# Kernel optimization log

Measured on AMD Instinct MI355X. Metric: run time of the kernel, lower is better.

## Reference

```python
import jax, jax.numpy as jnp
import numpy as np
import math

BS, H, L, D = 4, 8, 1024, 64
P = 513  # max_path_num + 1


def setup_inputs() -> dict:
    key = jax.random.key(0)
    ks = jax.random.split(key, 6)
    return {
        "query": jax.random.normal(ks[0], (BS, H, L, D), dtype=jnp.float32),
        "key": jax.random.normal(ks[1], (BS, H, L, D), dtype=jnp.float32),
        "value": jax.random.normal(ks[2], (BS, H, L, D), dtype=jnp.float32),
        "relation": jax.random.normal(ks[3], (BS, P, D), dtype=jnp.float32),
        "path_map": jax.random.randint(ks[4], (BS, L, L), 0, P, dtype=jnp.int32),
        "mask": jax.random.randint(ks[5], (BS, 1, L, L), 0, 2, dtype=jnp.int32),
    }


def reference(query, key, value, relation, path_map, mask):
    bs, h, Lc, d = query.shape
    p = relation.shape[1]
    # content score: bs,h,L,L
    score = jnp.einsum("bhik,bhjk->bhij", query, key)
    # relation score. Torch gathers with index of shape (bs,1,L,L) from a
    # (bs,h,L,P) tensor, which reads head 0 only and broadcasts over heads.
    score_r_h0 = jnp.einsum("bik,bpk->bip", query[:, 0], relation)  # bs,L,P
    gathered = jnp.take_along_axis(score_r_h0, path_map, axis=-1)   # bs,L,L
    score = score + gathered[:, None, :, :]
    scores = score / math.sqrt(d)
    scores = jnp.where(mask == 0, jnp.float32(-1e9), scores)
    p_attn = jax.nn.softmax(scores, axis=-1)  # bs,h,L,L
    attn_sum = jnp.einsum("bhij,bhjk->bhik", p_attn, value)
    # scatter-add attention probs into relation buckets: bs,h,L,P
    b_ix = jnp.arange(bs)[:, None, None, None]
    h_ix = jnp.arange(h)[None, :, None, None]
    i_ix = jnp.arange(Lc)[None, None, :, None]
    pm = jnp.broadcast_to(path_map[:, None, :, :], (bs, h, Lc, Lc))
    r_buckets = jnp.zeros((bs, h, Lc, p), dtype=p_attn.dtype).at[b_ix, h_ix, i_ix, pm].add(p_attn)
    r_attn_sum = jnp.einsum("bhip,bpk->bhik", r_buckets, relation)
    attn_sum = attn_sum + r_attn_sum
    return (attn_sum, p_attn)
```

## Files before the change

### kernel.cpp

```cpp
#include <hip/hip_runtime.h>


#define BSZ 4
#define NH 8
#define LSEQ 1024
#define DH 64
#define NP 513
#define TI 16
#define NT 1024
#define SRX 545
#define RTC 544

#define NQE (BSZ*NH*LSEQ*DH)
#define NRE (BSZ*NP*DH)
#define NRT (BSZ*DH*RTC)
#define OFF_QH 0
#define OFF_QL (NQE)
#define OFF_KH (2*NQE)
#define OFF_KL (3*NQE)
#define OFF_VT (4*NQE)
#define OFF_RH (5*NQE)
#define OFF_RL (5*NQE + NRE)
#define OFF_RT (5*NQE + 2*NRE)
#define WS_NEED ((size_t)(5*(size_t)NQE + 2*(size_t)NRE + (size_t)NRT) * 2)

typedef __attribute__((ext_vector_type(8))) short bf16x8;
typedef __attribute__((ext_vector_type(4))) float f32x4;
typedef __attribute__((ext_vector_type(4))) ushort u16x4;

__device__ __forceinline__ ushort f2bf(float x) {
    uint u = __float_as_uint(x);
    u += 0x7FFFu + ((u >> 16) & 1u);
    return (ushort)(u >> 16);
}
__device__ __forceinline__ float bf2f(ushort h) {
    return __uint_as_float(((uint)h) << 16);
}


__global__ void prep_qk(const float* __restrict__ Q, const float* __restrict__ K,
                        ushort* __restrict__ ws) {
    const int n4 = NQE / 4;
    for (int i = blockIdx.x * blockDim.x + threadIdx.x; i < 2 * n4;
         i += gridDim.x * blockDim.x) {
        int isK = i >= n4;
        int base = i - isK * n4;
        float4 v = ((const float4*)(isK ? K : Q))[base];
        float xs[4] = {v.x, v.y, v.z, v.w};
        u16x4 hh, ll;
        #pragma unroll
        for (int e = 0; e < 4; ++e) {
            ushort hi = f2bf(xs[e]);
            hh[e] = hi;
            ll[e] = f2bf(xs[e] - bf2f(hi));
        }
        *(u16x4*)(ws + (isK ? OFF_KH : OFF_QH) + (size_t)base * 4) = hh;
        *(u16x4*)(ws + (isK ? OFF_KL : OFF_QL) + (size_t)base * 4) = ll;
    }
}

__global__ void prep_rel(const float* __restrict__ REL, ushort* __restrict__ ws) {
    const int tot = NRE + NRT;
    for (int i = blockIdx.x * blockDim.x + threadIdx.x; i < tot;
         i += gridDim.x * blockDim.x) {
        if (i < NRE) {
            float x = REL[i];
            ushort hi = f2bf(x);
            ws[OFF_RH + i] = hi;
            ws[OFF_RL + i] = f2bf(x - bf2f(hi));
        } else {
            int j = i - NRE;
            int b = j / (DH * RTC);
            int r = j - b * (DH * RTC);
            int d = r / RTC;
            int p = r - d * RTC;
            float x = (p < NP) ? REL[((size_t)b * NP + p) * DH + d] : 0.f;
            ws[OFF_RT + j] = f2bf(x);
        }
    }
}

__global__ void prep_vt(const float* __restrict__ V, ushort* __restrict__ ws) {
    for (int i = blockIdx.x * blockDim.x + threadIdx.x; i < NQE;
         i += gridDim.x * blockDim.x) {
        int bh = i >> 16;
        int r  = i & 65535;
        int d  = r >> 10;
        int j  = r & 1023;
        ws[OFF_VT + (size_t)i] = f2bf(V[((size_t)bh << 16) + (j << 6) + d]);
    }
}


__global__ __launch_bounds__(NT, 4) void raa_main(
    const ushort* __restrict__ ws,
    const int* __restrict__ PM, const int* __restrict__ MASK,
    float* __restrict__ OUT_A, float* __restrict__ OUT_P)
{
    __shared__ float  X[TI * SRX];
    __shared__ ushort sPb[TI * 1024];
    __shared__ float  sAttn[TI * DH];
    __shared__ float  sRed[16 * 17];
    __shared__ float  sFin[16];

    const int tid = threadIdx.x;
    const int w  = tid >> 6;
    const int l  = tid & 63;
    const int lg = l >> 4;
    const int lm = l & 15;

    const int it = blockIdx.x, h = blockIdx.y, b = blockIdx.z;
    const int i0 = it * TI;
    const int bh = b * NH + h;

    const ushort* Qh  = ws + OFF_QH + (size_t)bh * LSEQ * DH;
    const ushort* Ql  = ws + OFF_QL + (size_t)bh * LSEQ * DH;
    const ushort* Q0h = ws + OFF_QH + (size_t)b * NH * LSEQ * DH;
    const ushort* Q0l = ws + OFF_QL + (size_t)b * NH * LSEQ * DH;
    const ushort* Kh  = ws + OFF_KH + (size_t)bh * LSEQ * DH;
    const ushort* Kl  = ws + OFF_KL + (size_t)bh * LSEQ * DH;
    const ushort* Vt  = ws + OFF_VT + (size_t)bh * DH * LSEQ;
    const ushort* Rh  = ws + OFF_RH + (size_t)b * NP * DH;
    const ushort* Rl  = ws + OFF_RL + (size_t)b * NP * DH;
    const ushort* Rt  = ws + OFF_RT + (size_t)b * DH * RTC;
    const int* PMb = PM + (size_t)b * LSEQ * LSEQ;
    const int* MKb = MASK + (size_t)b * LSEQ * LSEQ;

    sAttn[tid] = 0.f;

    bf16x8 q0h[2], q0l[2], qhh[2], qhl[2];
    #pragma unroll
    for (int ks = 0; ks < 2; ++ks) {
        size_t ao = (size_t)(i0 + lm) * DH + ks * 32 + lg * 8;
        q0h[ks] = *(const bf16x8*)(Q0h + ao);
        q0l[ks] = *(const bf16x8*)(Q0l + ao);
        qhh[ks] = *(const bf16x8*)(Qh + ao);
        qhl[ks] = *(const bf16x8*)(Ql + ao);
    }

    int pmr[16], mkr[16];
    #pragma unroll
    for (int t = 0; t < 4; ++t) {
        #pragma unroll
        for (int e = 0; e < 4; ++e) {
            int col = (4 * w + t) * 16 + lm;
            int row = 4 * lg + e;
            size_t off = (size_t)(i0 + row) * LSEQ + col;
            pmr[t * 4 + e] = PMb[off];
            mkr[t * 4 + e] = MKb[off];
        }
    }

    for (int ct = w; ct < 33; ct += 16) {
        int p0 = ct * 16;
        int prow = p0 + lm; if (prow > 512) prow = 512;
        f32x4 a0 = {0.f, 0.f, 0.f, 0.f};
        #pragma unroll
        for (int ks = 0; ks < 2; ++ks) {
            size_t bo = (size_t)prow * DH + ks * 32 + lg * 8;
            bf16x8 bh8 = *(const bf16x8*)(Rh + bo);
            bf16x8 bl8 = *(const bf16x8*)(Rl + bo);
            a0 = __builtin_amdgcn_mfma_f32_16x16x32_bf16(q0h[ks], bh8, a0, 0, 0, 0);
            a0 = __builtin_amdgcn_mfma_f32_16x16x32_bf16(q0l[ks], bh8, a0, 0, 0, 0);
            a0 = __builtin_amdgcn_mfma_f32_16x16x32_bf16(q0h[ks], bl8, a0, 0, 0, 0);
        }
        if (p0 + lm < NP) {
            #pragma unroll
            for (int e = 0; e < 4; ++e)
                X[(4 * lg + e) * SRX + p0 + lm] = a0[e];
        }
    }

    f32x4 acc[4];
    #pragma unroll
    for (int t = 0; t < 4; ++t) {
        int j0 = (4 * w + t) * 16;
        acc[t] = (f32x4){0.f, 0.f, 0.f, 0.f};
        #pragma unroll
        for (int ks = 0; ks < 2; ++ks) {
            size_t bo = (size_t)(j0 + lm) * DH + ks * 32 + lg * 8;
            bf16x8 kh8 = *(const bf16x8*)(Kh + bo);
            bf16x8 kl8 = *(const bf16x8*)(Kl + bo);
            acc[t] = __builtin_amdgcn_mfma_f32_16x16x32_bf16(qhh[ks], kh8, acc[t], 0, 0, 0);
            acc[t] = __builtin_amdgcn_mfma_f32_16x16x32_bf16(qhl[ks], kh8, acc[t], 0, 0, 0);
            acc[t] = __builtin_amdgcn_mfma_f32_16x16x32_bf16(qhh[ks], kl8, acc[t], 0, 0, 0);
        }
    }
    __syncthreads();

    #pragma unroll
    for (int t = 0; t < 4; ++t) {
        #pragma unroll
        for (int e = 0; e < 4; ++e) {
            int row = 4 * lg + e;
            float g = X[row * SRX + pmr[t * 4 + e]];
            acc[t][e] = (mkr[t * 4 + e] == 0) ? -1e9f : (acc[t][e] + g) * 0.125f;
        }
    }
    __syncthreads();
    for (int idx = tid; idx < TI * SRX; idx += NT) X[idx] = 0.f;
    __syncthreads();

    float Mr[4];
    #pragma unroll
    for (int e = 0; e < 4; ++e) {
        float m = fmaxf(fmaxf(acc[0][e], acc[1][e]), fmaxf(acc[2][e], acc[3][e]));
        #pragma unroll
        for (int o = 8; o >= 1; o >>= 1) m = fmaxf(m, __shfl_xor(m, o));
        Mr[e] = m;
    }
    if (lm == 0) {
        #pragma unroll
        for (int e = 0; e < 4; ++e) sRed[(4 * lg + e) * 17 + w] = Mr[e];
    }
    __syncthreads();
    if (w == 0 && l < 16) {
        float m = -INFINITY;
        for (int ww = 0; ww < 16; ++ww) m = fmaxf(m, sRed[l * 17 + ww]);
        sFin[l] = m;
    }
    __syncthreads();
    #pragma unroll
    for (int e = 0; e < 4; ++e) Mr[e] = sFin[4 * lg + e];

    float Sr[4];
    #pragma unroll
    for (int e = 0; e < 4; ++e) {
        float s = 0.f;
        #pragma unroll
        for (int t = 0; t < 4; ++t) {
            float v = __expf(acc[t][e] - Mr[e]);
            acc[t][e] = v;
            s += v;
        }
        #pragma unroll
        for (int o = 8; o >= 1; o >>= 1) s += __shfl_xor(s, o);
        Sr[e] = s;
    }
    if (lm == 0) {
        #pragma unroll
        for (int e = 0; e < 4; ++e) sRed[(4 * lg + e) * 17 + w] = Sr[e];
    }
    __syncthreads();
    if (w == 0 && l < 16) {
        float s = 0.f;
        for (int ww = 0; ww < 16; ++ww) s += sRed[l * 17 + ww];
        sFin[l] = s;
    }
    __syncthreads();

    float inv[4];
    #pragma unroll
    for (int e = 0; e < 4; ++e) inv[e] = 1.0f / sFin[4 * lg + e];

    const size_t pbase = (((size_t)bh) * LSEQ + i0) * LSEQ;
    #pragma unroll
    for (int t = 0; t < 4; ++t) {
        int col = (4 * w + t) * 16 + lm;
        #pragma unroll
        for (int e = 0; e < 4; ++e) {
            int row = 4 * lg + e;
            float p = acc[t][e] * inv[e];
            OUT_P[pbase + (size_t)row * LSEQ + col] = p;
            sPb[row * 1024 + (((col >> 3) ^ (row & 7)) << 3) + (col & 7)] = f2bf(p);
            atomicAdd(&X[row * SRX + pmr[t * 4 + e]], p);
        }
    }
    __syncthreads();

    if (w < 8) {
        int ct = w >> 1, jh = w & 1;
        int d0 = ct * 16;
        f32x4 pa = {0.f, 0.f, 0.f, 0.f};
        #pragma unroll 4
        for (int ks = 0; ks < 16; ++ks) {
            int j0 = jh * 512 + ks * 32;
            int ch = (j0 >> 3) + lg;
            bf16x8 a = *(const bf16x8*)&sPb[lm * 1024 + ((ch ^ (lm & 7)) << 3)];
            bf16x8 bb = *(const bf16x8*)(Vt + (size_t)(d0 + lm) * LSEQ + j0 + lg * 8);
            pa = __builtin_amdgcn_mfma_f32_16x16x32_bf16(a, bb, pa, 0, 0, 0);
        }
        #pragma unroll
        for (int e = 0; e < 4; ++e)
            atomicAdd(&sAttn[(4 * lg + e) * DH + d0 + lm], pa[e]);
    } else {
        int ct = (w - 8) >> 1, ph = w & 1;
        int d0 = ct * 16;
        int nks = ph ? 8 : 9;
        int pb0 = ph ? 288 : 0;
        f32x4 pa = {0.f, 0.f, 0.f, 0.f};
        for (int ks = 0; ks < nks; ++ks) {
            int p0 = pb0 + ks * 32;
            bf16x8 a;
            #pragma unroll
            for (int e = 0; e < 8; ++e)
                a[e] = (short)f2bf(X[lm * SRX + p0 + lg * 8 + e]);
            bf16x8 bb = *(const bf16x8*)(Rt + (size_t)(d0 + lm) * RTC + p0 + lg * 8);
            pa = __builtin_amdgcn_mfma_f32_16x16x32_bf16(a, bb, pa, 0, 0, 0);
        }
        #pragma unroll
        for (int e = 0; e < 4; ++e)
            atomicAdd(&sAttn[(4 * lg + e) * DH + d0 + lm], pa[e]);
    }
    __syncthreads();

    OUT_A[(((size_t)bh) * LSEQ + i0 + (tid >> 6)) * DH + (tid & 63)] = sAttn[tid];
}


__global__ __launch_bounds__(NT, 4) void raa_fallback(
    const float* __restrict__ Q, const float* __restrict__ K,
    const float* __restrict__ V, const float* __restrict__ REL,
    const int* __restrict__ PM, const int* __restrict__ MASK,
    float* __restrict__ OUT_A, float* __restrict__ OUT_P)
{
    __shared__ ushort sQh[TI * 64];
    __shared__ ushort sQl[TI * 64];
    __shared__ float  sR[TI * NP];
    __shared__ ushort sPb[TI * 1024];
    __shared__ float  sAttn[TI * 64];
    __shared__ float  sRed[16 * 17];
    __shared__ float  sFin[16];

    const int tid = threadIdx.x;
    const int w  = tid >> 6;
    const int l  = tid & 63;
    const int lg = l >> 4;
    const int lm = l & 15;

    const int it = blockIdx.x, h = blockIdx.y, b = blockIdx.z;
    const int i0 = it * TI;

    const float* Qb0  = Q + ((size_t)b * NH + 0) * LSEQ * DH;
    const float* Qbh  = Q + ((size_t)b * NH + h) * LSEQ * DH;
    const float* Kbh  = K + ((size_t)b * NH + h) * LSEQ * DH;
    const float* Vbh  = V + ((size_t)b * NH + h) * LSEQ * DH;
    const float* RELb = REL + (size_t)b * NP * DH;
    const int*   PMb  = PM  + (size_t)b * LSEQ * LSEQ;
    const int*   MKb  = MASK + (size_t)b * LSEQ * LSEQ;

    {
        int row = tid >> 6, kk = tid & 63;
        float x = Qb0[(size_t)(i0 + row) * DH + kk];
        ushort hi = f2bf(x);
        ushort lo = f2bf(x - bf2f(hi));
        int ad = row * 64 + (((kk >> 3) ^ (row & 7)) << 3) + (kk & 7);
        sQh[ad] = hi; sQl[ad] = lo;
        sAttn[tid] = 0.f;
    }
    __syncthreads();

    bf16x8 qh[2], ql[2];
    #pragma unroll
    for (int ks = 0; ks < 2; ++ks) {
        int ch = lg + 4 * ks;
        int ad = lm * 64 + ((ch ^ (lm & 7)) << 3);
        qh[ks] = *(const bf16x8*)&sQh[ad];
        ql[ks] = *(const bf16x8*)&sQl[ad];
    }
    __syncthreads();

    {
        int row = tid >> 6, kk = tid & 63;
        float x = Qbh[(size_t)(i0 + row) * DH + kk];
        ushort hi = f2bf(x);
        ushort lo = f2bf(x - bf2f(hi));
        int ad = row * 64 + (((kk >> 3) ^ (row & 7)) << 3) + (kk & 7);
        sQh[ad] = hi; sQl[ad] = lo;
    }

    for (int ct = w; ct < 33; ct += 16) {
        int p0 = ct * 16;
        int prow = p0 + lm; if (prow > 512) prow = 512;
        const float* bsrc = RELb + (size_t)prow * DH + 8 * lg;
        f32x4 acc = {0.f, 0.f, 0.f, 0.f};
        #pragma unroll
        for (int ks = 0; ks < 2; ++ks) {
            float4 v0 = *(const float4*)(bsrc + ks * 32);
            float4 v1 = *(const float4*)(bsrc + ks * 32 + 4);
            float xs[8] = {v0.x, v0.y, v0.z, v0.w, v1.x, v1.y, v1.z, v1.w};
            bf16x8 bh, bl;
            #pragma unroll
            for (int e = 0; e < 8; ++e) {
                ushort hi = f2bf(xs[e]);
                bh[e] = (short)hi;
                bl[e] = (short)f2bf(xs[e] - bf2f(hi));
            }
            acc = __builtin_amdgcn_mfma_f32_16x16x32_bf16(qh[ks], bh, acc, 0, 0, 0);
            acc = __builtin_amdgcn_mfma_f32_16x16x32_bf16(ql[ks], bh, acc, 0, 0, 0);
            acc = __builtin_amdgcn_mfma_f32_16x16x32_bf16(qh[ks], bl, acc, 0, 0, 0);
        }
        int pcol = p0 + lm;
        if (pcol < NP) {
            #pragma unroll
            for (int e = 0; e < 4; ++e)
                sR[(4 * lg + e) * NP + pcol] = acc[e];
        }
    }
    __syncthreads();

    {
        int ad0;
        #pragma unroll
        for (int ks = 0; ks < 2; ++ks) {
            int ch = lg + 4 * ks;
            ad0 = lm * 64 + ((ch ^ (lm & 7)) << 3);
            qh[ks] = *(const bf16x8*)&sQh[ad0];
            ql[ks] = *(const bf16x8*)&sQl[ad0];
        }
    }
    f32x4 acc[4];
    #pragma unroll
    for (int t = 0; t < 4; ++t) {
        int j = (4 * w + t) * 16 + lm;
        const float* bsrc = Kbh + (size_t)j * DH + 8 * lg;
        acc[t] = (f32x4){0.f, 0.f, 0.f, 0.f};
        #pragma unroll
        for (int ks = 0; ks < 2; ++ks) {
            float4 v0 = *(const float4*)(bsrc + ks * 32);
            float4 v1 = *(const float4*)(bsrc + ks * 32 + 4);
            float xs[8] = {v0.x, v0.y, v0.z, v0.w, v1.x, v1.y, v1.z, v1.w};
            bf16x8 bh, bl;
            #pragma unroll
            for (int e = 0; e < 8; ++e) {
                ushort hi = f2bf(xs[e]);
                bh[e] = (short)hi;
                bl[e] = (short)f2bf(xs[e] - bf2f(hi));
            }
            acc[t] = __builtin_amdgcn_mfma_f32_16x16x32_bf16(qh[ks], bh, acc[t], 0, 0, 0);
            acc[t] = __builtin_amdgcn_mfma_f32_16x16x32_bf16(ql[ks], bh, acc[t], 0, 0, 0);
            acc[t] = __builtin_amdgcn_mfma_f32_16x16x32_bf16(qh[ks], bl, acc[t], 0, 0, 0);
        }
    }

    #pragma unroll
    for (int t = 0; t < 4; ++t) {
        int col = (4 * w + t) * 16 + lm;
        #pragma unroll
        for (int e = 0; e < 4; ++e) {
            int row = 4 * lg + e;
            size_t off = (size_t)(i0 + row) * LSEQ + col;
            int pm = PMb[off];
            int mk = MKb[off];
            float g = sR[row * NP + pm];
            acc[t][e] = (mk == 0) ? -1e9f : (acc[t][e] + g) * 0.125f;
        }
    }
    __syncthreads();
    for (int idx = tid; idx < TI * NP; idx += NT) sR[idx] = 0.f;
    __syncthreads();

    float Mr[4];
    #pragma unroll
    for (int e = 0; e < 4; ++e) {
        float m = fmaxf(fmaxf(acc[0][e], acc[1][e]), fmaxf(acc[2][e], acc[3][e]));
        #pragma unroll
        for (int o = 8; o >= 1; o >>= 1) m = fmaxf(m, __shfl_xor(m, o));
        Mr[e] = m;
    }
    if (lm == 0) {
        #pragma unroll
        for (int e = 0; e < 4; ++e) sRed[(4 * lg + e) * 17 + w] = Mr[e];
    }
    __syncthreads();
    if (w == 0 && l < 16) {
        float m = -INFINITY;
        for (int ww = 0; ww < 16; ++ww) m = fmaxf(m, sRed[l * 17 + ww]);
        sFin[l] = m;
    }
    __syncthreads();
    #pragma unroll
    for (int e = 0; e < 4; ++e) Mr[e] = sFin[4 * lg + e];

    float Sr[4];
    #pragma unroll
    for (int e = 0; e < 4; ++e) {
        float s = 0.f;
        #pragma unroll
        for (int t = 0; t < 4; ++t) {
            float v = __expf(acc[t][e] - Mr[e]);
            acc[t][e] = v;
            s += v;
        }
        #pragma unroll
        for (int o = 8; o >= 1; o >>= 1) s += __shfl_xor(s, o);
        Sr[e] = s;
    }
    if (lm == 0) {
        #pragma unroll
        for (int e = 0; e < 4; ++e) sRed[(4 * lg + e) * 17 + w] = Sr[e];
    }
    __syncthreads();
    if (w == 0 && l < 16) {
        float s = 0.f;
        for (int ww = 0; ww < 16; ++ww) s += sRed[l * 17 + ww];
        sFin[l] = s;
    }
    __syncthreads();

    float inv[4];
    #pragma unroll
    for (int e = 0; e < 4; ++e) inv[e] = 1.0f / sFin[4 * lg + e];

    const size_t pbase = (((size_t)b * NH + h) * LSEQ + i0) * LSEQ;
    #pragma unroll
    for (int t = 0; t < 4; ++t) {
        int col = (4 * w + t) * 16 + lm;
        #pragma unroll
        for (int e = 0; e < 4; ++e) {
            int row = 4 * lg + e;
            float p = acc[t][e] * inv[e];
            OUT_P[pbase + (size_t)row * LSEQ + col] = p;
            int ad = row * 1024 + (((col >> 3) ^ (row & 7)) << 3) + (col & 7);
            sPb[ad] = f2bf(p);
            int pm = PMb[(size_t)(i0 + row) * LSEQ + col];
            atomicAdd(&sR[row * NP + pm], p);
        }
    }
    __syncthreads();

    if (w < 8) {
        int ct = w >> 1, jh = w & 1;
        int d = ct * 16 + lm;
        f32x4 pa = {0.f, 0.f, 0.f, 0.f};
        for (int ks = 0; ks < 16; ++ks) {
            int j0 = jh * 512 + ks * 32;
            int ch = (j0 >> 3) + lg;
            bf16x8 a = *(const bf16x8*)&sPb[lm * 1024 + ((ch ^ (lm & 7)) << 3)];
            const float* vs = Vbh + (size_t)(j0 + 8 * lg) * DH + d;
            bf16x8 bb;
            #pragma unroll
            for (int e = 0; e < 8; ++e) bb[e] = (short)f2bf(vs[(size_t)e * DH]);
            pa = __builtin_amdgcn_mfma_f32_16x16x32_bf16(a, bb, pa, 0, 0, 0);
        }
        #pragma unroll
        for (int e = 0; e < 4; ++e)
            atomicAdd(&sAttn[(4 * lg + e) * 64 + d], pa[e]);
    } else {
        int ct = (w - 8) >> 1, ph = w & 1;
        int d = ct * 16 + lm;
        int nks = ph ? 9 : 8;
        f32x4 pa = {0.f, 0.f, 0.f, 0.f};
        for (int ks = 0; ks < nks; ++ks) {
            int p0 = ph * 256 + ks * 32 + 8 * lg;
            bf16x8 a, bb;
            #pragma unroll
            for (int e = 0; e < 8; ++e) {
                int pp = p0 + e;
                float av = (pp < NP) ? sR[lm * NP + pp] : 0.f;
                a[e] = (short)f2bf(av);
                int pc = (pp < NP) ? pp : (NP - 1);
                bb[e] = (short)f2bf(RELb[(size_t)pc * DH + d]);
            }
            pa = __builtin_amdgcn_mfma_f32_16x16x32_bf16(a, bb, pa, 0, 0, 0);
        }
        #pragma unroll
        for (int e = 0; e < 4; ++e)
            atomicAdd(&sAttn[(4 * lg + e) * 64 + d], pa[e]);
    }
    __syncthreads();

    {
        int row = tid >> 6, col = tid & 63;
        OUT_A[(((size_t)b * NH + h) * LSEQ + i0 + row) * DH + col] =
            sAttn[row * 64 + col];
    }
}

extern "C" void kernel_launch(void* const* d_in, const int* in_sizes, int n_in,
                              void* d_out, int out_size, void* d_ws, size_t ws_size,
                              hipStream_t stream) {
    const float* q    = (const float*)d_in[0];
    const float* k    = (const float*)d_in[1];
    const float* v    = (const float*)d_in[2];
    const float* rel  = (const float*)d_in[3];
    const int*   pm   = (const int*)d_in[4];
    const int*   mask = (const int*)d_in[5];
    float* out_a = (float*)d_out;
    float* out_p = (float*)d_out + (size_t)BSZ * NH * LSEQ * DH;

    dim3 grid(LSEQ / TI, NH, BSZ);
    if (ws_size >= WS_NEED && d_ws != nullptr) {
        ushort* ws = (ushort*)d_ws;
        prep_qk<<<2048, 256, 0, stream>>>(q, k, ws);
        prep_rel<<<512, 256, 0, stream>>>(rel, ws);
        prep_vt<<<2048, 256, 0, stream>>>(v, ws);
        raa_main<<<grid, NT, 0, stream>>>((const ushort*)ws, pm, mask, out_a, out_p);
    } else {
        raa_fallback<<<grid, NT, 0, stream>>>(q, k, v, rel, pm, mask, out_a, out_p);
    }
}
```

Baseline: 585.8 us.

## Precompute relation scores once per batch and streamline softmax and output stores

```diff
diff --git a/kernel.cpp b/kernel.cpp
--- a/kernel.cpp
+++ b/kernel.cpp
@@ -12,17 +12,16 @@
 #define RTC 544
 
 #define NQE (BSZ*NH*LSEQ*DH)
-#define NRE (BSZ*NP*DH)
 #define NRT (BSZ*DH*RTC)
+#define NSR (BSZ*LSEQ*NP)
 #define OFF_QH 0
 #define OFF_QL (NQE)
 #define OFF_KH (2*NQE)
 #define OFF_KL (3*NQE)
 #define OFF_VT (4*NQE)
-#define OFF_RH (5*NQE)
-#define OFF_RL (5*NQE + NRE)
-#define OFF_RT (5*NQE + 2*NRE)
-#define WS_NEED ((size_t)(5*(size_t)NQE + 2*(size_t)NRE + (size_t)NRT) * 2)
+#define OFF_RT (5*NQE)
+#define OFF_SR (5*NQE + NRT)
+#define WS_NEED ((size_t)(5*(size_t)NQE + (size_t)NRT + (size_t)NSR) * 2)
 
 typedef __attribute__((ext_vector_type(8))) short bf16x8;
 typedef __attribute__((ext_vector_type(4))) float f32x4;
@@ -59,35 +58,89 @@
     }
 }
 
-__global__ void prep_rel(const float* __restrict__ REL, ushort* __restrict__ ws) {
-    const int tot = NRE + NRT;
-    for (int i = blockIdx.x * blockDim.x + threadIdx.x; i < tot;
+__global__ void prep_rt(const float* __restrict__ REL, ushort* __restrict__ ws) {
+    for (int i = blockIdx.x * blockDim.x + threadIdx.x; i < NRT;
          i += gridDim.x * blockDim.x) {
-        if (i < NRE) {
-            float x = REL[i];
-            ushort hi = f2bf(x);
-            ws[OFF_RH + i] = hi;
-            ws[OFF_RL + i] = f2bf(x - bf2f(hi));
-        } else {
-            int j = i - NRE;
-            int b = j / (DH * RTC);
-            int r = j - b * (DH * RTC);
-            int d = r / RTC;
-            int p = r - d * RTC;
-            float x = (p < NP) ? REL[((size_t)b * NP + p) * DH + d] : 0.f;
-            ws[OFF_RT + j] = f2bf(x);
-        }
-    }
-}
-
-__global__ void prep_vt(const float* __restrict__ V, ushort* __restrict__ ws) {
-    for (int i = blockIdx.x * blockDim.x + threadIdx.x; i < NQE;
-         i += gridDim.x * blockDim.x) {
-        int bh = i >> 16;
-        int r  = i & 65535;
-        int d  = r >> 10;
-        int j  = r & 1023;
-        ws[OFF_VT + (size_t)i] = f2bf(V[((size_t)bh << 16) + (j << 6) + d]);
+        int b = i / (DH * RTC);
+        int r = i - b * (DH * RTC);
+        int d = r / RTC;
+        int p = r - d * RTC;
+        float x = (p < NP) ? REL[((size_t)b * NP + p) * DH + d] : 0.f;
+        ws[OFF_RT + i] = f2bf(x);
+    }
+}
+
+__global__ __launch_bounds__(256) void prep_vt(const float* __restrict__ V,
+                                               ushort* __restrict__ ws) {
+    __shared__ float sT[64 * 65];
+    const int bh = blockIdx.y;
+    const int j0 = blockIdx.x * 64;
+    const float* Vb = V + ((size_t)bh << 16);
+    for (int i = threadIdx.x; i < 1024; i += 256) {
+        int jr = i >> 4, c4 = i & 15;
+        float4 vv = *(const float4*)(Vb + (size_t)(j0 + jr) * DH + c4 * 4);
+        float* dst = &sT[jr * 65 + c4 * 4];
+        dst[0] = vv.x; dst[1] = vv.y; dst[2] = vv.z; dst[3] = vv.w;
+    }
+    __syncthreads();
+    const int d = threadIdx.x >> 2, jseg = threadIdx.x & 3;
+    ushort* dst = ws + OFF_VT + ((size_t)bh << 16) + (size_t)d * LSEQ + j0 + jseg * 16;
+    #pragma unroll
+    for (int g = 0; g < 4; ++g) {
+        u16x4 o;
+        #pragma unroll
+        for (int e = 0; e < 4; ++e)
+            o[e] = f2bf(sT[(jseg * 16 + g * 4 + e) * 65 + d]);
+        *(u16x4*)(dst + g * 4) = o;
+    }
+}
+
+__global__ __launch_bounds__(256) void prep_sr(const float* __restrict__ REL,
+                                               ushort* __restrict__ ws) {
+    const int tid = threadIdx.x;
+    const int w = tid >> 6, l = tid & 63, lg = l >> 4, lm = l & 15;
+    const int it = blockIdx.x, b = blockIdx.y;
+    const int i0 = it * TI;
+
+    const ushort* Qh = ws + OFF_QH + (size_t)b * NH * LSEQ * DH;
+    const ushort* Ql = ws + OFF_QL + (size_t)b * NH * LSEQ * DH;
+    const float* RELb = REL + (size_t)b * NP * DH;
+    ushort* SRb = ws + OFF_SR + (size_t)b * LSEQ * NP;
+
+    bf16x8 qh[2], ql[2];
+    #pragma unroll
+    for (int ks = 0; ks < 2; ++ks) {
+        size_t ao = (size_t)(i0 + lm) * DH + ks * 32 + lg * 8;
+        qh[ks] = *(const bf16x8*)(Qh + ao);
+        ql[ks] = *(const bf16x8*)(Ql + ao);
+    }
+
+    for (int ct = w; ct < 33; ct += 4) {
+        int p0 = ct * 16;
+        int prow = p0 + lm; if (prow > 512) prow = 512;
+        f32x4 a0 = {0.f, 0.f, 0.f, 0.f};
+        #pragma unroll
+        for (int ks = 0; ks < 2; ++ks) {
+            const float* bsrc = RELb + (size_t)prow * DH + ks * 32 + lg * 8;
+            float4 v0 = *(const float4*)(bsrc);
+            float4 v1 = *(const float4*)(bsrc + 4);
+            float xs[8] = {v0.x, v0.y, v0.z, v0.w, v1.x, v1.y, v1.z, v1.w};
+            bf16x8 bh8, bl8;
+            #pragma unroll
+            for (int e = 0; e < 8; ++e) {
+                ushort hi = f2bf(xs[e]);
+                bh8[e] = (short)hi;
+                bl8[e] = (short)f2bf(xs[e] - bf2f(hi));
+            }
+            a0 = __builtin_amdgcn_mfma_f32_16x16x32_bf16(qh[ks], bh8, a0, 0, 0, 0);
+            a0 = __builtin_amdgcn_mfma_f32_16x16x32_bf16(ql[ks], bh8, a0, 0, 0, 0);
+            a0 = __builtin_amdgcn_mfma_f32_16x16x32_bf16(qh[ks], bl8, a0, 0, 0, 0);
+        }
+        if (p0 + lm < NP) {
+            #pragma unroll
+            for (int e = 0; e < 4; ++e)
+                SRb[(size_t)(i0 + 4 * lg + e) * NP + p0 + lm] = f2bf(a0[e]);
+        }
     }
 }
 
@@ -100,8 +153,8 @@
     __shared__ float  X[TI * SRX];
     __shared__ ushort sPb[TI * 1024];
     __shared__ float  sAttn[TI * DH];
-    __shared__ float  sRed[16 * 17];
-    __shared__ float  sFin[16];
+    __shared__ float  sRedM[16 * 17];
+    __shared__ float  sRedS[16 * 17];
 
     const int tid = threadIdx.x;
     const int w  = tid >> 6;
@@ -113,160 +166,151 @@
     const int i0 = it * TI;
     const int bh = b * NH + h;
 
-    const ushort* Qh  = ws + OFF_QH + (size_t)bh * LSEQ * DH;
-    const ushort* Ql  = ws + OFF_QL + (size_t)bh * LSEQ * DH;
-    const ushort* Q0h = ws + OFF_QH + (size_t)b * NH * LSEQ * DH;
-    const ushort* Q0l = ws + OFF_QL + (size_t)b * NH * LSEQ * DH;
-    const ushort* Kh  = ws + OFF_KH + (size_t)bh * LSEQ * DH;
-    const ushort* Kl  = ws + OFF_KL + (size_t)bh * LSEQ * DH;
-    const ushort* Vt  = ws + OFF_VT + (size_t)bh * DH * LSEQ;
-    const ushort* Rh  = ws + OFF_RH + (size_t)b * NP * DH;
-    const ushort* Rl  = ws + OFF_RL + (size_t)b * NP * DH;
-    const ushort* Rt  = ws + OFF_RT + (size_t)b * DH * RTC;
+    const ushort* Qh = ws + OFF_QH + (size_t)bh * LSEQ * DH;
+    const ushort* Ql = ws + OFF_QL + (size_t)bh * LSEQ * DH;
+    const ushort* Kh = ws + OFF_KH + (size_t)bh * LSEQ * DH;
+    const ushort* Kl = ws + OFF_KL + (size_t)bh * LSEQ * DH;
+    const ushort* Vt = ws + OFF_VT + (size_t)bh * DH * LSEQ;
+    const ushort* Rt = ws + OFF_RT + (size_t)b * DH * RTC;
+    const ushort* SRb = ws + OFF_SR + (size_t)b * LSEQ * NP;
     const int* PMb = PM + (size_t)b * LSEQ * LSEQ;
     const int* MKb = MASK + (size_t)b * LSEQ * LSEQ;
 
+    #pragma unroll
+    for (int z = 0; z < 9; ++z) {
+        int idx = z * NT + tid;
+        if (idx < TI * SRX) X[idx] = 0.f;
+    }
     sAttn[tid] = 0.f;
 
-    bf16x8 q0h[2], q0l[2], qhh[2], qhl[2];
+    int pmr[16];
+    float gf[16];
+    {
+        int mk[16]; ushort gu[16];
+        #pragma unroll
+        for (int t = 0; t < 4; ++t) {
+            #pragma unroll
+            for (int e = 0; e < 4; ++e) {
+                int col = (4 * w + t) * 16 + lm;
+                int row = 4 * lg + e;
+                size_t off = (size_t)(i0 + row) * LSEQ + col;
+                pmr[t * 4 + e] = PMb[off];
+                mk[t * 4 + e]  = MKb[off];
+            }
+        }
+        #pragma unroll
+        for (int i = 0; i < 16; ++i) {
+            int row = 4 * lg + (i & 3);
+            gu[i] = SRb[(size_t)(i0 + row) * NP + pmr[i]];
+        }
+        #pragma unroll
+        for (int i = 0; i < 16; ++i)
+            gf[i] = mk[i] ? bf2f(gu[i]) : -3e38f;
+    }
+
+    bf16x8 qhh[2], qhl[2];
     #pragma unroll
     for (int ks = 0; ks < 2; ++ks) {
         size_t ao = (size_t)(i0 + lm) * DH + ks * 32 + lg * 8;
-        q0h[ks] = *(const bf16x8*)(Q0h + ao);
-        q0l[ks] = *(const bf16x8*)(Q0l + ao);
         qhh[ks] = *(const bf16x8*)(Qh + ao);
         qhl[ks] = *(const bf16x8*)(Ql + ao);
     }
 
-    int pmr[16], mkr[16];
+    f32x4 acc[4];
+    bf16x8 kh_c[2], kl_c[2], kh_n[2], kl_n[2];
+    {
+        size_t bo = (size_t)(4 * w * 16 + lm) * DH + lg * 8;
+        kh_c[0] = *(const bf16x8*)(Kh + bo);      kl_c[0] = *(const bf16x8*)(Kl + bo);
+        kh_c[1] = *(const bf16x8*)(Kh + bo + 32); kl_c[1] = *(const bf16x8*)(Kl + bo + 32);
+    }
     #pragma unroll
     for (int t = 0; t < 4; ++t) {
+        if (t < 3) {
+            size_t bo = (size_t)((4 * w + t + 1) * 16 + lm) * DH + lg * 8;
+            kh_n[0] = *(const bf16x8*)(Kh + bo);      kl_n[0] = *(const bf16x8*)(Kl + bo);
+            kh_n[1] = *(const bf16x8*)(Kh + bo + 32); kl_n[1] = *(const bf16x8*)(Kl + bo + 32);
+        }
+        acc[t] = (f32x4){0.f, 0.f, 0.f, 0.f};
+        #pragma unroll
+        for (int ks = 0; ks < 2; ++ks) {
+            acc[t] = __builtin_amdgcn_mfma_f32_16x16x32_bf16(qhh[ks], kh_c[ks], acc[t], 0, 0, 0);
+            acc[t] = __builtin_amdgcn_mfma_f32_16x16x32_bf16(qhl[ks], kh_c[ks], acc[t], 0, 0, 0);
+            acc[t] = __builtin_amdgcn_mfma_f32_16x16x32_bf16(qhh[ks], kl_c[ks], acc[t], 0, 0, 0);
+        }
+        #pragma unroll
+        for (int ks = 0; ks < 2; ++ks) {
+            kh_c[ks] = kh_n[ks]; kl_c[ks] = kl_n[ks];
+        }
+    }
+
+    #pragma unroll
+    for (int t = 0; t < 4; ++t) {
         #pragma unroll
         for (int e = 0; e < 4; ++e) {
-            int col = (4 * w + t) * 16 + lm;
-            int row = 4 * lg + e;
-            size_t off = (size_t)(i0 + row) * LSEQ + col;
-            pmr[t * 4 + e] = PMb[off];
-            mkr[t * 4 + e] = MKb[off];
-        }
-    }
-
-    for (int ct = w; ct < 33; ct += 16) {
-        int p0 = ct * 16;
-        int prow = p0 + lm; if (prow > 512) prow = 512;
-        f32x4 a0 = {0.f, 0.f, 0.f, 0.f};
-        #pragma unroll
-        for (int ks = 0; ks < 2; ++ks) {
-            size_t bo = (size_t)prow * DH + ks * 32 + lg * 8;
-            bf16x8 bh8 = *(const bf16x8*)(Rh + bo);
-            bf16x8 bl8 = *(const bf16x8*)(Rl + bo);
-            a0 = __builtin_amdgcn_mfma_f32_16x16x32_bf16(q0h[ks], bh8, a0, 0, 0, 0);
-            a0 = __builtin_amdgcn_mfma_f32_16x16x32_bf16(q0l[ks], bh8, a0, 0, 0, 0);
-            a0 = __builtin_amdgcn_mfma_f32_16x16x32_bf16(q0h[ks], bl8, a0, 0, 0, 0);
-        }
-        if (p0 + lm < NP) {
-            #pragma unroll
-            for (int e = 0; e < 4; ++e)
-                X[(4 * lg + e) * SRX + p0 + lm] = a0[e];
-        }
-    }
-
-    f32x4 acc[4];
+            float g = gf[t * 4 + e];
+            acc[t][e] = (g < -1e30f) ? -1e9f : (acc[t][e] + g) * 0.125f;
+        }
+    }
+
+    float mw[4], c4v[4];
+    #pragma unroll
+    for (int e = 0; e < 4; ++e) {
+        float m = fmaxf(fmaxf(acc[0][e], acc[1][e]), fmaxf(acc[2][e], acc[3][e]));
+        #pragma unroll
+        for (int o = 8; o >= 1; o >>= 1) m = fmaxf(m, __shfl_xor(m, o));
+        mw[e] = m;
+        float s = 0.f;
+        #pragma unroll
+        for (int t = 0; t < 4; ++t) {
+            float v = __expf(acc[t][e] - m);
+            acc[t][e] = v;
+            s += v;
+        }
+        #pragma unroll
+        for (int o = 8; o >= 1; o >>= 1) s += __shfl_xor(s, o);
+        if (lm == 0) {
+            sRedM[(4 * lg + e) * 17 + w] = m;
+            sRedS[(4 * lg + e) * 17 + w] = s;
+        }
+    }
+    __syncthreads();
+    #pragma unroll
+    for (int e = 0; e < 4; ++e) {
+        int row = 4 * lg + e;
+        float mv = sRedM[row * 17 + lm];
+        float sv = sRedS[row * 17 + lm];
+        float m = mv;
+        #pragma unroll
+        for (int o = 8; o >= 1; o >>= 1) m = fmaxf(m, __shfl_xor(m, o));
+        float sp = sv * __expf(mv - m);
+        #pragma unroll
+        for (int o = 8; o >= 1; o >>= 1) sp += __shfl_xor(sp, o);
+        c4v[e] = __expf(mw[e] - m) / sp;
+    }
+
     #pragma unroll
     for (int t = 0; t < 4; ++t) {
-        int j0 = (4 * w + t) * 16;
-        acc[t] = (f32x4){0.f, 0.f, 0.f, 0.f};
-        #pragma unroll
-        for (int ks = 0; ks < 2; ++ks) {
-            size_t bo = (size_t)(j0 + lm) * DH + ks * 32 + lg * 8;
-            bf16x8 kh8 = *(const bf16x8*)(Kh + bo);
-            bf16x8 kl8 = *(const bf16x8*)(Kl + bo);
-            acc[t] = __builtin_amdgcn_mfma_f32_16x16x32_bf16(qhh[ks], kh8, acc[t], 0, 0, 0);
-            acc[t] = __builtin_amdgcn_mfma_f32_16x16x32_bf16(qhl[ks], kh8, acc[t], 0, 0, 0);
-            acc[t] = __builtin_amdgcn_mfma_f32_16x16x32_bf16(qhh[ks], kl8, acc[t], 0, 0, 0);
-        }
-    }
-    __syncthreads();
-
-    #pragma unroll
-    for (int t = 0; t < 4; ++t) {
+        int col = (4 * w + t) * 16 + lm;
         #pragma unroll
         for (int e = 0; e < 4; ++e) {
             int row = 4 * lg + e;
-            float g = X[row * SRX + pmr[t * 4 + e]];
-            acc[t][e] = (mkr[t * 4 + e] == 0) ? -1e9f : (acc[t][e] + g) * 0.125f;
-        }
-    }
-    __syncthreads();
-    for (int idx = tid; idx < TI * SRX; idx += NT) X[idx] = 0.f;
-    __syncthreads();
-
-    float Mr[4];
-    #pragma unroll
-    for (int e = 0; e < 4; ++e) {
-        float m = fmaxf(fmaxf(acc[0][e], acc[1][e]), fmaxf(acc[2][e], acc[3][e]));
-        #pragma unroll
-        for (int o = 8; o >= 1; o >>= 1) m = fmaxf(m, __shfl_xor(m, o));
-        Mr[e] = m;
-    }
-    if (lm == 0) {
-        #pragma unroll
-        for (int e = 0; e < 4; ++e) sRed[(4 * lg + e) * 17 + w] = Mr[e];
-    }
-    __syncthreads();
-    if (w == 0 && l < 16) {
-        float m = -INFINITY;
-        for (int ww = 0; ww < 16; ++ww) m = fmaxf(m, sRed[l * 17 + ww]);
-        sFin[l] = m;
-    }
-    __syncthreads();
-    #pragma unroll
-    for (int e = 0; e < 4; ++e) Mr[e] = sFin[4 * lg + e];
-
-    float Sr[4];
-    #pragma unroll
-    for (int e = 0; e < 4; ++e) {
-        float s = 0.f;
-        #pragma unroll
-        for (int t = 0; t < 4; ++t) {
-            float v = __expf(acc[t][e] - Mr[e]);
-            acc[t][e] = v;
-            s += v;
-        }
-        #pragma unroll
-        for (int o = 8; o >= 1; o >>= 1) s += __shfl_xor(s, o);
-        Sr[e] = s;
-    }
-    if (lm == 0) {
-        #pragma unroll
-        for (int e = 0; e < 4; ++e) sRed[(4 * lg + e) * 17 + w] = Sr[e];
-    }
-    __syncthreads();
-    if (w == 0 && l < 16) {
-        float s = 0.f;
-        for (int ww = 0; ww < 16; ++ww) s += sRed[l * 17 + ww];
-        sFin[l] = s;
-    }
-    __syncthreads();
-
-    float inv[4];
-    #pragma unroll
-    for (int e = 0; e < 4; ++e) inv[e] = 1.0f / sFin[4 * lg + e];
-
-    const size_t pbase = (((size_t)bh) * LSEQ + i0) * LSEQ;
-    #pragma unroll
-    for (int t = 0; t < 4; ++t) {
-        int col = (4 * w + t) * 16 + lm;
-        #pragma unroll
-        for (int e = 0; e < 4; ++e) {
-            int row = 4 * lg + e;
-            float p = acc[t][e] * inv[e];
-            OUT_P[pbase + (size_t)row * LSEQ + col] = p;
+            float p = acc[t][e] * c4v[e];
             sPb[row * 1024 + (((col >> 3) ^ (row & 7)) << 3) + (col & 7)] = f2bf(p);
             atomicAdd(&X[row * SRX + pmr[t * 4 + e]], p);
         }
     }
     __syncthreads();
+
+    const size_t pbase = ((size_t)bh * LSEQ + i0) * LSEQ;
+    #pragma unroll
+    for (int g = 0; g < 4; ++g) {
+        int elem = g * 4096 + tid * 4;
+        int r = elem >> 10, cc = elem & 1023;
+        int ad = r * 1024 + (((cc >> 3) ^ (r & 7)) << 3) + (cc & 7);
+        u16x4 pv = *(const u16x4*)&sPb[ad];
+        float4 o4 = make_float4(bf2f(pv[0]), bf2f(pv[1]), bf2f(pv[2]), bf2f(pv[3]));
+        *(float4*)(OUT_P + pbase + (size_t)r * LSEQ + cc) = o4;
+    }
 
     if (w < 8) {
         int ct = w >> 1, jh = w & 1;
@@ -304,7 +348,7 @@
     }
     __syncthreads();
 
-    OUT_A[(((size_t)bh) * LSEQ + i0 + (tid >> 6)) * DH + (tid & 63)] = sAttn[tid];
+    OUT_A[((size_t)bh * LSEQ + i0 + (tid >> 6)) * DH + (tid & 63)] = sAttn[tid];
 }
 
 
@@ -399,15 +443,12 @@
     }
     __syncthreads();
 
-    {
-        int ad0;
-        #pragma unroll
-        for (int ks = 0; ks < 2; ++ks) {
-            int ch = lg + 4 * ks;
-            ad0 = lm * 64 + ((ch ^ (lm & 7)) << 3);
-            qh[ks] = *(const bf16x8*)&sQh[ad0];
-            ql[ks] = *(const bf16x8*)&sQl[ad0];
-        }
+    #pragma unroll
+    for (int ks = 0; ks < 2; ++ks) {
+        int ch = lg + 4 * ks;
+        int ad = lm * 64 + ((ch ^ (lm & 7)) << 3);
+        qh[ks] = *(const bf16x8*)&sQh[ad];
+        ql[ks] = *(const bf16x8*)&sQl[ad];
     }
     f32x4 acc[4];
     #pragma unroll
@@ -583,8 +624,9 @@
     if (ws_size >= WS_NEED && d_ws != nullptr) {
         ushort* ws = (ushort*)d_ws;
         prep_qk<<<2048, 256, 0, stream>>>(q, k, ws);
-        prep_rel<<<512, 256, 0, stream>>>(rel, ws);
-        prep_vt<<<2048, 256, 0, stream>>>(v, ws);
+        prep_vt<<<dim3(16, 32), 256, 0, stream>>>(v, ws);
+        prep_rt<<<256, 256, 0, stream>>>(rel, ws);
+        prep_sr<<<dim3(LSEQ / TI, BSZ), 256, 0, stream>>>(rel, ws);
         raa_main<<<grid, NT, 0, stream>>>((const ushort*)ws, pm, mask, out_a, out_p);
     } else {
         raa_fallback<<<grid, NT, 0, stream>>>(q, k, v, rel, pm, mask, out_a, out_p);
```

Measured after the change: 569.1 us. 2.9% less time.
